# Optimization experiments

Measured on AMD Instinct MI355X. Metric: run time of the kernel, lower is better.

Reference implementation:

```python
import jax, jax.numpy as jnp
import numpy as np

H = 128  # GRU hidden size

def gru_cell(x, h, Wih, Whh, bih, bhh):
    # torch GRU gate order: r, z, n
    gx = x @ Wih.T + bih          # (B, 3H)
    gh = h @ Whh.T + bhh          # (B, 3H)
    xr, xz, xn = jnp.split(gx, 3, axis=-1)
    hr, hz, hn = jnp.split(gh, 3, axis=-1)
    r = jax.nn.sigmoid(xr + hr)
    z = jax.nn.sigmoid(xz + hz)
    n = jnp.tanh(xn + r * hn)
    return (1.0 - z) * n + z * h

def conv2d(x, w, b, stride):
    y = jax.lax.conv_general_dilated(x, w, window_strides=(stride, stride), padding='VALID',
                                     dimension_numbers=('NCHW', 'OIHW', 'NCHW'))
    return y + b[None, :, None, None]

def setup_inputs() -> dict:
    key = jax.random.key(0)
    ks = jax.random.split(key, 20)
    B, T = 8192, 64
    s = lambda *sh: 0.1
    inp = {
        'cnn_states': jax.random.normal(ks[0], (B, 8, 8, 27), jnp.float32),
        'linears_states': jax.random.normal(ks[1], (B, T, 29), jnp.float32),
        'conv1_w': jax.random.normal(ks[2], (16, 27, 3, 3), jnp.float32) * 0.1,
        'conv1_b': jnp.zeros((16,), jnp.float32),
        'conv2_w': jax.random.normal(ks[3], (32, 16, 2, 2), jnp.float32) * 0.1,
        'conv2_b': jnp.zeros((32,), jnp.float32),
        'fc_w': jax.random.normal(ks[4], (128, 128), jnp.float32) * 0.1,
        'fc_b': jnp.zeros((128,), jnp.float32),
        'enc_Wih': jax.random.normal(ks[5], (3 * H, 29), jnp.float32) * 0.1,
        'enc_Whh': jax.random.normal(ks[6], (3 * H, H), jnp.float32) * 0.1,
        'enc_bih': jnp.zeros((3 * H,), jnp.float32),
        'enc_bhh': jnp.zeros((3 * H,), jnp.float32),
        'dec_Wih': jax.random.normal(ks[7], (3 * H, H), jnp.float32) * 0.1,
        'dec_Whh': jax.random.normal(ks[8], (3 * H, H), jnp.float32) * 0.1,
        'dec_bih': jnp.zeros((3 * H,), jnp.float32),
        'dec_bhh': jnp.zeros((3 * H,), jnp.float32),
        'dis_w': jax.random.normal(ks[9], (78, 256), jnp.float32) * 0.01,
        'dis_b': jnp.zeros((78,), jnp.float32),
        'value_w': jax.random.normal(ks[10], (1, 256), jnp.float32) * 0.1,
        'value_b': jnp.zeros((1,), jnp.float32),
    }
    return inp

def _forward(cnn_states, linears_states, conv1_w, conv1_b, conv2_w, conv2_b, fc_w, fc_b,
             enc_Wih, enc_Whh, enc_bih, enc_bhh, dec_Wih, dec_Whh, dec_bih, dec_bhh,
             dis_w, dis_b, value_w, value_b):
    B, T = linears_states.shape[0], linears_states.shape[1]
    # CNN encoder (NHWC -> NCHW)
    x = jnp.transpose(cnn_states, (0, 3, 1, 2))
    x = jax.nn.relu(conv2d(x, conv1_w, conv1_b, 2))   # (B,16,3,3)
    x = jax.nn.relu(conv2d(x, conv2_w, conv2_b, 1))   # (B,32,2,2)
    x = x.reshape(B, -1)                               # (B,128), CHW order matches torch Flatten
    z_cnn = jax.nn.relu(x @ fc_w.T + fc_b)             # (B,128)

    # encoder GRU over linears_states
    xs = jnp.transpose(linears_states, (1, 0, 2))      # (T,B,29)
    h0 = jnp.zeros((B, H), linears_states.dtype)
    def enc_step(h, xt):
        h2 = gru_cell(xt, h, enc_Wih, enc_Whh, enc_bih, enc_bhh)
        return h2, None
    h_enc, _ = jax.lax.scan(enc_step, h0, xs)

    x0 = jnp.zeros((B, H), linears_states.dtype)
    def dec_step(carry, _):
        xin, h = carry
        h2 = gru_cell(xin, h, dec_Wih, dec_Whh, dec_bih, dec_bhh)
        return (h2, h2), None
    (z_pn, _), _ = jax.lax.scan(dec_step, (x0, h_enc), None, length=T)

    pn = jnp.concatenate([z_cnn, z_pn], axis=1)        # (B,256)
    distris = pn @ dis_w.T + dis_b                     # (B,78)
    value = pn @ value_w.T + value_b                   # (B,1)
    return distris, value

def reference(cnn_states, linears_states, conv1_w, conv1_b, conv2_w, conv2_b, fc_w, fc_b,
              enc_Wih, enc_Whh, enc_bih, enc_bhh, dec_Wih, dec_Whh, dec_bih, dec_bhh,
              dis_w, dis_b, value_w, value_b):
    return _forward(cnn_states, linears_states, conv1_w, conv1_b, conv2_w, conv2_b, fc_w, fc_b,
                    enc_Wih, enc_Whh, enc_bih, enc_bhh, dec_Wih, dec_Whh, dec_bih, dec_bhh,
                    dis_w, dis_b, value_w, value_b)
```

## Files before the change

### kernel.cpp

```cpp
#include <hip/hip_runtime.h>

typedef _Float16 f16;
typedef _Float16 f16x8 __attribute__((ext_vector_type(8)));
typedef float f32x4 __attribute__((ext_vector_type(4)));

#define WS_ZCNN 0
#define WS_EWIH 4194304
#define WS_EWHH 4218880
#define WS_DWC  4317184
#define WS_DWHH 4448256
#define WS_BIAS 4546560
#define WS_W1F  4550656
#define WS_W2F  4559872
#define WS_FCWF 4563968

static __device__ __forceinline__ f32x4 mfma16(f16x8 a, f16x8 b, f32x4 c) {
    return __builtin_amdgcn_mfma_f32_16x16x32_f16(a, b, c, 0, 0, 0);
}
static __device__ __forceinline__ float fexp2n(float x) {
    return __builtin_amdgcn_exp2f(x * -1.4426950408889634f);
}
static __device__ __forceinline__ void pin(f16x8& x) { asm volatile("" : "+v"(x)); }

__global__ void k_prep(const float* __restrict__ eWih, const float* __restrict__ eWhh,
                       const float* __restrict__ ebih, const float* __restrict__ ebhh,
                       const float* __restrict__ dWih, const float* __restrict__ dWhh,
                       const float* __restrict__ dbih, const float* __restrict__ dbhh,
                       const float* __restrict__ w1, const float* __restrict__ w2,
                       const float* __restrict__ fcw,
                       char* __restrict__ ws)
{
    f16* ewih = (f16*)(ws + WS_EWIH);
    f16* ewhh = (f16*)(ws + WS_EWHH);
    f16* dwc  = (f16*)(ws + WS_DWC);
    f16* dwhh = (f16*)(ws + WS_DWHH);
    float* bias = (float*)(ws + WS_BIAS);
    f16* w1f = (f16*)(ws + WS_W1F);
    f16* w2f = (f16*)(ws + WS_W2F);
    f16* fcwf = (f16*)(ws + WS_FCWF);
    const int total = 12288 + 49152 + 65536 + 49152 + 1024 + 4608 + 2048 + 16384;
    for (int i = blockIdx.x * 256 + threadIdx.x; i < total; i += gridDim.x * 256) {
        int j = i;
        if (j < 12288) { int g = j >> 5, k = j & 31;
            ewih[j] = (f16)((k < 29) ? eWih[g * 29 + k] : 0.0f); continue; }
        j -= 12288;
        if (j < 49152) { ewhh[j] = (f16)eWhh[j]; continue; }
        j -= 49152;
        if (j < 65536) { int row = j >> 7, k = j & 127; float v;
            if (row < 256)      v = dWih[row * 128 + k] + dWhh[row * 128 + k];
            else if (row < 384) v = dWih[row * 128 + k];
            else                v = dWhh[(row - 128) * 128 + k];
            dwc[j] = (f16)v; continue; }
        j -= 65536;
        if (j < 49152) { dwhh[j] = (f16)dWhh[j]; continue; }
        j -= 49152;
        if (j < 1024) {
            if (j < 256)        bias[j] = ebih[j] + ebhh[j];
            else if (j < 384)   bias[j] = ebih[j];
            else if (j < 512)   bias[j] = ebhh[j - 128];
            else if (j < 768)   bias[j] = dbih[j - 512] + dbhh[j - 512];
            else if (j < 896)   bias[j] = dbih[j - 512];
            else                bias[j] = dbhh[j - 640];
            continue; }
        j -= 1024;
        if (j < 4608) {
            int kk = j >> 9, rem = j & 511, co = rem >> 5, k = rem & 31;
            w1f[j] = (f16)((k < 27) ? w1[co * 243 + k * 9 + kk] : 0.0f); continue; }
        j -= 4608;
        if (j < 2048) {
            int s = j >> 10, rem = j & 1023, co = rem >> 5, k = rem & 31;
            int kk2 = 2 * s + (k >= 16), ci = k & 15;
            w2f[j] = (f16)w2[co * 64 + ci * 4 + kk2]; continue; }
        j -= 2048;
        fcwf[j] = (f16)fcw[j];
    }
}

__global__ __launch_bounds__(256) void k_cnn(
    const float* __restrict__ cin,
    const float* __restrict__ b1, const float* __restrict__ b2,
    const float* __restrict__ fcb,
    char* __restrict__ ws)
{
    __shared__ __align__(16) f16 a1f[16][9][24];
    __shared__ __align__(16) f16 vf[16][136];

    const int tid = threadIdx.x;
    const int base = blockIdx.x * 16;
    const f16* w1f = (const f16*)(ws + WS_W1F);
    const f16* w2f = (const f16*)(ws + WS_W2F);
    const f16* fcwf = (const f16*)(ws + WS_FCWF);
    float* z = (float*)(ws + WS_ZCNN);

    const int wv = tid >> 6, lane = tid & 63, nl = lane & 15, quad = lane >> 4;

    f16x8 bw1[9];
    #pragma unroll
    for (int kk = 0; kk < 9; kk++)
        bw1[kk] = *(const f16x8*)(w1f + (kk * 16 + nl) * 32 + quad * 8);
    float b1v = b1[nl];
    const float* imgp = cin + (size_t)(base + nl) * 1728 + quad * 8;
    for (int p = wv; p < 9; p += 4) {
        int oy = p / 3, ox = p % 3;
        f32x4 acc = {b1v, b1v, b1v, b1v};
        #pragma unroll
        for (int kk = 0; kk < 9; kk++) {
            int pix = (2 * oy + kk / 3) * 8 + (2 * ox + kk % 3);
            const float* s = imgp + pix * 27;
            f16x8 a;
            #pragma unroll
            for (int jj = 0; jj < 8; jj++) a[jj] = (f16)s[jj];
            acc = mfma16(a, bw1[kk], acc);
        }
        #pragma unroll
        for (int r = 0; r < 4; r++)
            a1f[quad * 4 + r][p][nl] = (f16)fmaxf(acc[r], 0.0f);
    }
    __syncthreads();

    {
        int y = wv >> 1, x = wv & 1;
        #pragma unroll
        for (int nt = 0; nt < 2; nt++) {
            float bv = b2[nt * 16 + nl];
            f32x4 acc = {bv, bv, bv, bv};
            #pragma unroll
            for (int s = 0; s < 2; s++) {
                int kk2 = 2 * s + (quad >> 1);
                int pos1 = (y + (kk2 >> 1)) * 3 + (x + (kk2 & 1));
                f16x8 a = *(const f16x8*)(&a1f[nl][pos1][(quad & 1) * 8]);
                f16x8 b = *(const f16x8*)(w2f + ((size_t)s * 32 + nt * 16 + nl) * 32 + quad * 8);
                acc = mfma16(a, b, acc);
            }
            #pragma unroll
            for (int r = 0; r < 4; r++)
                vf[quad * 4 + r][(nt * 16 + nl) * 4 + (y * 2 + x)] = (f16)fmaxf(acc[r], 0.0f);
        }
    }
    __syncthreads();

    #pragma unroll
    for (int nt = 0; nt < 2; nt++) {
        int o = wv * 32 + nt * 16 + nl;
        float bv = fcb[o];
        f32x4 acc = {bv, bv, bv, bv};
        #pragma unroll
        for (int kt = 0; kt < 4; kt++) {
            f16x8 a = *(const f16x8*)(&vf[nl][kt * 32 + quad * 8]);
            f16x8 b = *(const f16x8*)(fcwf + o * 128 + kt * 32 + quad * 8);
            acc = mfma16(a, b, acc);
        }
        #pragma unroll
        for (int r = 0; r < 4; r++)
            z[(size_t)(base + quad * 4 + r) * 128 + o] = fmaxf(acc[r], 0.0f);
    }
}

__global__ __launch_bounds__(512, 4) void k_gru(
    const float* __restrict__ lin,
    const char* __restrict__ ws,
    const float* __restrict__ dis_w, const float* __restrict__ dis_b,
    const float* __restrict__ value_w, const float* __restrict__ value_b,
    float* __restrict__ out)
{
    const int tid = threadIdx.x;
    const int wv = tid >> 6;
    const int lane = tid & 63;
    const int nl = lane & 15;
    const int quad = lane >> 4;
    const int j0 = wv * 16;
    const int row0 = blockIdx.x * 16;

    const f16* ewih = (const f16*)(ws + WS_EWIH);
    const f16* ewhh = (const f16*)(ws + WS_EWHH);
    const f16* dwc  = (const f16*)(ws + WS_DWC);
    const f16* dwhh = (const f16*)(ws + WS_DWHH);
    const float* bias = (const float*)(ws + WS_BIAS);
    const float* z_cnn = (const float*)(ws + WS_ZCNN);

    __shared__ __align__(16) f16 h_s[2][16][136];
    __shared__ __align__(16) f16 x_s[2][16][32];
    __shared__ __align__(16) float pn_s[16][264];

    for (int i = tid; i < 2 * 16 * 136; i += 512) ((f16*)h_s)[i] = (f16)0.0f;

    const int rsw = (nl & 8) ? 16 : 0;
    const int wrow = quad * 4;
    const int wsw = (quad >= 2) ? 16 : 0;
    const int wcol = (j0 + nl + wsw) & 127;
    const int c0 = (quad * 8 + rsw) & 127;
    const int c1 = (32 + quad * 8 + rsw) & 127;
    const int c2 = (64 + quad * 8 + rsw) & 127;
    const int c3 = (96 + quad * 8 + rsw) & 127;

    float ho[4];
    #pragma unroll
    for (int r = 0; r < 4; r++) ho[r] = 0.0f;

    const int xr = tid >> 5, xc = tid & 31;
    const bool xok = (xc < 29);
    const size_t lin_base = (size_t)(row0 + xr) * 1856 + xc;

    {
        float eb_r, eb_z, eb_xn, eb_hn;
        { int c = j0 + nl;
          eb_r = bias[c]; eb_z = bias[128 + c]; eb_xn = bias[256 + c]; eb_hn = bias[384 + c]; }
        f16x8 we_r[4], we_z[4], we_hn[4], we_xr, we_xz, we_xn;
        { int gr = j0 + nl;
          #pragma unroll
          for (int kt = 0; kt < 4; kt++) {
              we_r[kt]  = *(const f16x8*)(ewhh + gr * 128 + kt * 32 + quad * 8);
              we_z[kt]  = *(const f16x8*)(ewhh + (128 + gr) * 128 + kt * 32 + quad * 8);
              we_hn[kt] = *(const f16x8*)(ewhh + (256 + gr) * 128 + kt * 32 + quad * 8);
              pin(we_r[kt]); pin(we_z[kt]); pin(we_hn[kt]);
          }
          we_xr = *(const f16x8*)(ewih + gr * 32 + quad * 8);
          we_xz = *(const f16x8*)(ewih + (128 + gr) * 32 + quad * 8);
          we_xn = *(const f16x8*)(ewih + (256 + gr) * 32 + quad * 8);
          pin(we_xr); pin(we_xz); pin(we_xn);
        }

        float xv = xok ? lin[lin_base] : 0.0f;

#define ENC_STEP(BUF, OBUF, TN)                                                      \
        do {                                                                         \
            x_s[BUF][xr][xc] = (f16)xv;                                              \
            __syncthreads();                                                         \
            f16x8 ax = *(const f16x8*)(&x_s[BUF][nl][quad * 8]);                     \
            f16x8 ah0 = *(const f16x8*)(&h_s[BUF][nl][c0]);                          \
            f16x8 ah1 = *(const f16x8*)(&h_s[BUF][nl][c1]);                          \
            f16x8 ah2 = *(const f16x8*)(&h_s[BUF][nl][c2]);                          \
            f16x8 ah3 = *(const f16x8*)(&h_s[BUF][nl][c3]);                          \
            if ((TN) < 64) xv = xok ? lin[lin_base + (TN) * 29] : 0.0f;              \
            f32x4 aR  = {eb_r, eb_r, eb_r, eb_r};                                    \
            f32x4 aZ  = {eb_z, eb_z, eb_z, eb_z};                                    \
            f32x4 aXN = {eb_xn, eb_xn, eb_xn, eb_xn};                                \
            f32x4 aHN = {eb_hn, eb_hn, eb_hn, eb_hn};                                \
            aR  = mfma16(ax, we_xr, aR);                                             \
            aZ  = mfma16(ax, we_xz, aZ);                                             \
            aXN = mfma16(ax, we_xn, aXN);                                            \
            aR  = mfma16(ah0, we_r[0], aR);  aR  = mfma16(ah1, we_r[1], aR);         \
            aR  = mfma16(ah2, we_r[2], aR);  aR  = mfma16(ah3, we_r[3], aR);         \
            aZ  = mfma16(ah0, we_z[0], aZ);  aZ  = mfma16(ah1, we_z[1], aZ);         \
            aZ  = mfma16(ah2, we_z[2], aZ);  aZ  = mfma16(ah3, we_z[3], aZ);         \
            aHN = mfma16(ah0, we_hn[0], aHN); aHN = mfma16(ah1, we_hn[1], aHN);      \
            aHN = mfma16(ah2, we_hn[2], aHN); aHN = mfma16(ah3, we_hn[3], aHN);      \
            _Pragma("unroll")                                                        \
            for (int r = 0; r < 4; r++) {                                            \
                float ea = fexp2n(aR[r]), eb = fexp2n(aZ[r]);                        \
                float s1 = 1.0f + ea, s2 = 1.0f + eb;                                \
                float R = __builtin_amdgcn_rcpf(s1 * s2);                            \
                float rg = s2 * R, zg = s1 * R;                                      \
                float ec = fexp2n(2.0f * (aXN[r] + rg * aHN[r]));                    \
                float ng = (1.0f - ec) * __builtin_amdgcn_rcpf(1.0f + ec);           \
                float h = (1.0f - zg) * ng + zg * ho[r];                             \
                ho[r] = h;                                                           \
                h_s[OBUF][wrow + r][wcol] = (f16)h;                                  \
            }                                                                        \
        } while (0)

        for (int t = 0; t < 64; t += 2) {
            ENC_STEP(0, 1, t + 1);
            ENC_STEP(1, 0, t + 2);
        }
#undef ENC_STEP
    }

    float db_r, db_z, db_xn, db_hn;
    { int c = j0 + nl;
      db_r = bias[512 + c]; db_z = bias[640 + c]; db_xn = bias[768 + c]; db_hn = bias[896 + c]; }

    {
        __syncthreads();
        f16x8 ah0 = *(const f16x8*)(&h_s[0][nl][c0]);
        f16x8 ah1 = *(const f16x8*)(&h_s[0][nl][c1]);
        f16x8 ah2 = *(const f16x8*)(&h_s[0][nl][c2]);
        f16x8 ah3 = *(const f16x8*)(&h_s[0][nl][c3]);
        int gr = j0 + nl;
        f32x4 aR  = {db_r, db_r, db_r, db_r};
        f32x4 aZ  = {db_z, db_z, db_z, db_z};
        f32x4 aHN = {db_hn, db_hn, db_hn, db_hn};
        #pragma unroll
        for (int kt = 0; kt < 4; kt++) {
            f16x8 b0 = *(const f16x8*)(dwhh + gr * 128 + kt * 32 + quad * 8);
            f16x8 b1 = *(const f16x8*)(dwhh + (128 + gr) * 128 + kt * 32 + quad * 8);
            f16x8 b2 = *(const f16x8*)(dwhh + (256 + gr) * 128 + kt * 32 + quad * 8);
            f16x8 a = (kt == 0) ? ah0 : (kt == 1) ? ah1 : (kt == 2) ? ah2 : ah3;
            aR  = mfma16(a, b0, aR);
            aZ  = mfma16(a, b1, aZ);
            aHN = mfma16(a, b2, aHN);
        }
        #pragma unroll
        for (int r = 0; r < 4; r++) {
            float ea = fexp2n(aR[r]), eb = fexp2n(aZ[r]);
            float s1 = 1.0f + ea, s2 = 1.0f + eb;
            float R = __builtin_amdgcn_rcpf(s1 * s2);
            float rg = s2 * R, zg = s1 * R;
            float ec = fexp2n(2.0f * (db_xn + rg * aHN[r]));
            float ng = (1.0f - ec) * __builtin_amdgcn_rcpf(1.0f + ec);
            float h = (1.0f - zg) * ng + zg * ho[r];
            ho[r] = h;
            h_s[1][wrow + r][wcol] = (f16)h;
        }
    }
    {
        f16x8 wd_r[4], wd_z[4], wd_xn[4], wd_hn[4];
        { int gr = j0 + nl;
          #pragma unroll
          for (int kt = 0; kt < 4; kt++) {
              wd_r[kt]  = *(const f16x8*)(dwc + gr * 128 + kt * 32 + quad * 8);
              wd_z[kt]  = *(const f16x8*)(dwc + (128 + gr) * 128 + kt * 32 + quad * 8);
              wd_xn[kt] = *(const f16x8*)(dwc + (256 + gr) * 128 + kt * 32 + quad * 8);
              wd_hn[kt] = *(const f16x8*)(dwc + (384 + gr) * 128 + kt * 32 + quad * 8);
              pin(wd_r[kt]); pin(wd_z[kt]); pin(wd_xn[kt]); pin(wd_hn[kt]);
          }
        }

#define DEC_STEP(BUF, OBUF)                                                          \
        do {                                                                         \
            __syncthreads();                                                         \
            f16x8 ah0 = *(const f16x8*)(&h_s[BUF][nl][c0]);                          \
            f16x8 ah1 = *(const f16x8*)(&h_s[BUF][nl][c1]);                          \
            f16x8 ah2 = *(const f16x8*)(&h_s[BUF][nl][c2]);                          \
            f16x8 ah3 = *(const f16x8*)(&h_s[BUF][nl][c3]);                          \
            f32x4 aR  = {db_r, db_r, db_r, db_r};                                    \
            f32x4 aZ  = {db_z, db_z, db_z, db_z};                                    \
            f32x4 aXN = {db_xn, db_xn, db_xn, db_xn};                                \
            f32x4 aHN = {db_hn, db_hn, db_hn, db_hn};                                \
            aR  = mfma16(ah0, wd_r[0], aR);   aR  = mfma16(ah1, wd_r[1], aR);        \
            aR  = mfma16(ah2, wd_r[2], aR);   aR  = mfma16(ah3, wd_r[3], aR);        \
            aZ  = mfma16(ah0, wd_z[0], aZ);   aZ  = mfma16(ah1, wd_z[1], aZ);        \
            aZ  = mfma16(ah2, wd_z[2], aZ);   aZ  = mfma16(ah3, wd_z[3], aZ);        \
            aXN = mfma16(ah0, wd_xn[0], aXN); aXN = mfma16(ah1, wd_xn[1], aXN);      \
            aXN = mfma16(ah2, wd_xn[2], aXN); aXN = mfma16(ah3, wd_xn[3], aXN);      \
            aHN = mfma16(ah0, wd_hn[0], aHN); aHN = mfma16(ah1, wd_hn[1], aHN);      \
            aHN = mfma16(ah2, wd_hn[2], aHN); aHN = mfma16(ah3, wd_hn[3], aHN);      \
            _Pragma("unroll")                                                        \
            for (int r = 0; r < 4; r++) {                                            \
                float ea = fexp2n(aR[r]), eb = fexp2n(aZ[r]);                        \
                float s1 = 1.0f + ea, s2 = 1.0f + eb;                                \
                float R = __builtin_amdgcn_rcpf(s1 * s2);                            \
                float rg = s2 * R, zg = s1 * R;                                      \
                float ec = fexp2n(2.0f * (aXN[r] + rg * aHN[r]));                    \
                float ng = (1.0f - ec) * __builtin_amdgcn_rcpf(1.0f + ec);           \
                float h = (1.0f - zg) * ng + zg * ho[r];                             \
                ho[r] = h;                                                           \
                h_s[OBUF][wrow + r][wcol] = (f16)h;                                  \
            }                                                                        \
        } while (0)

        DEC_STEP(1, 0);
        for (int t = 2; t < 64; t += 2) {
            DEC_STEP(0, 1);
            DEC_STEP(1, 0);
        }
#undef DEC_STEP
    }

    #pragma unroll
    for (int r = 0; r < 4; r++)
        pn_s[wrow + r][128 + j0 + nl] = ho[r];
    for (int i = tid; i < 16 * 128; i += 512) {
        int rr = i >> 7, cc = i & 127;
        pn_s[rr][cc] = z_cnn[(size_t)(row0 + rr) * 128 + cc];
    }
    __syncthreads();

    const int rr = tid & 15, og = tid >> 4;
    const float4* pr4 = (const float4*)(&pn_s[rr][0]);
    for (int o = og; o < 79; o += 32) {
        const float* wrow_p = (o < 78) ? (dis_w + o * 256) : value_w;
        float acc = (o < 78) ? dis_b[o] : value_b[0];
        const float4* wr4 = (const float4*)wrow_p;
        #pragma unroll 8
        for (int k = 0; k < 64; k++) {
            float4 a = wr4[k], b = pr4[k];
            acc += a.x * b.x + a.y * b.y + a.z * b.z + a.w * b.w;
        }
        if (o < 78) out[(size_t)(row0 + rr) * 78 + o] = acc;
        else        out[(size_t)8192 * 78 + row0 + rr] = acc;
    }
}

extern "C" void kernel_launch(void* const* d_in, const int* in_sizes, int n_in,
                              void* d_out, int out_size, void* d_ws, size_t ws_size,
                              hipStream_t stream)
{
    (void)in_sizes; (void)n_in; (void)out_size; (void)ws_size;
    const float* cnn  = (const float*)d_in[0];
    const float* lin  = (const float*)d_in[1];
    const float* c1w  = (const float*)d_in[2];
    const float* c1b  = (const float*)d_in[3];
    const float* c2w  = (const float*)d_in[4];
    const float* c2b  = (const float*)d_in[5];
    const float* fcw  = (const float*)d_in[6];
    const float* fcb  = (const float*)d_in[7];
    const float* eWih = (const float*)d_in[8];
    const float* eWhh = (const float*)d_in[9];
    const float* ebih = (const float*)d_in[10];
    const float* ebhh = (const float*)d_in[11];
    const float* dWih = (const float*)d_in[12];
    const float* dWhh = (const float*)d_in[13];
    const float* dbih = (const float*)d_in[14];
    const float* dbhh = (const float*)d_in[15];
    const float* disw = (const float*)d_in[16];
    const float* disb = (const float*)d_in[17];
    const float* vw   = (const float*)d_in[18];
    const float* vb   = (const float*)d_in[19];
    char* ws = (char*)d_ws;
    float* out = (float*)d_out;

    hipLaunchKernelGGL(k_prep, dim3(128), dim3(256), 0, stream,
                       eWih, eWhh, ebih, ebhh, dWih, dWhh, dbih, dbhh,
                       c1w, c2w, fcw, ws);
    hipLaunchKernelGGL(k_cnn, dim3(512), dim3(256), 0, stream,
                       cnn, c1b, c2b, fcb, ws);
    hipLaunchKernelGGL(k_gru, dim3(512), dim3(512), 0, stream,
                       lin, ws, disw, disb, vw, vb, out);
}
```

Before: 350.0 us.

## Fuse CNN branch into GRU kernel and write CNN features directly to shared memory

The separate CNN kernel is folded into the start of the GRU kernel. Its conv1, conv2 and fc stages run over 8 waves with aliased shared memory, and the fc output is written straight into the pn_s buffer, which removes the global round trip of z_cnn and one kernel launch. The asm register-pinning barriers on the weight fragments are dropped, and the GRU state update is rewritten as ng + z*(h-ng) to save an operation. The cost is that CNN work now adds latency to each GRU block, and conv1 uses only 9 of 8x2 wave slots, which leaves some waves idle. It also risks different register allocation in the GRU loop now that the pins are gone.

```diff
diff --git a/kernel.cpp b/kernel.cpp
--- a/kernel.cpp
+++ b/kernel.cpp
@@ -4,7 +4,6 @@
 typedef _Float16 f16x8 __attribute__((ext_vector_type(8)));
 typedef float f32x4 __attribute__((ext_vector_type(4)));
 
-#define WS_ZCNN 0
 #define WS_EWIH 4194304
 #define WS_EWHH 4218880
 #define WS_DWC  4317184
@@ -20,7 +19,6 @@
 static __device__ __forceinline__ float fexp2n(float x) {
     return __builtin_amdgcn_exp2f(x * -1.4426950408889634f);
 }
-static __device__ __forceinline__ void pin(f16x8& x) { asm volatile("" : "+v"(x)); }
 
 __global__ void k_prep(const float* __restrict__ eWih, const float* __restrict__ eWhh,
                        const float* __restrict__ ebih, const float* __restrict__ ebhh,
@@ -76,52 +74,64 @@
     }
 }
 
-__global__ __launch_bounds__(256) void k_cnn(
+__global__ __launch_bounds__(512, 4) void k_gru(
     const float* __restrict__ cin,
+    const float* __restrict__ lin,
     const float* __restrict__ b1, const float* __restrict__ b2,
     const float* __restrict__ fcb,
-    char* __restrict__ ws)
+    const char* __restrict__ ws,
+    const float* __restrict__ dis_w, const float* __restrict__ dis_b,
+    const float* __restrict__ value_w, const float* __restrict__ value_b,
+    float* __restrict__ out)
 {
-    __shared__ __align__(16) f16 a1f[16][9][24];
-    __shared__ __align__(16) f16 vf[16][136];
+    __shared__ __align__(16) char smem[32000];
+    f16 (*h_s)[16][136]  = (f16(*)[16][136])(smem);
+    f16 (*x_s)[16][32]   = (f16(*)[16][32])(smem + 8704);
+    float (*pn_s)[264]   = (float(*)[264])(smem + 10752);
+    f16 (*a1f)[9][24]    = (f16(*)[9][24])(smem);
+    f16 (*vf)[136]       = (f16(*)[136])(smem + 27648);
 
     const int tid = threadIdx.x;
-    const int base = blockIdx.x * 16;
+    const int wv = tid >> 6;
+    const int lane = tid & 63;
+    const int nl = lane & 15;
+    const int quad = lane >> 4;
+    const int j0 = wv * 16;
+    const int row0 = blockIdx.x * 16;
+
+    const f16* ewih = (const f16*)(ws + WS_EWIH);
+    const f16* ewhh = (const f16*)(ws + WS_EWHH);
+    const f16* dwc  = (const f16*)(ws + WS_DWC);
+    const f16* dwhh = (const f16*)(ws + WS_DWHH);
+    const float* bias = (const float*)(ws + WS_BIAS);
     const f16* w1f = (const f16*)(ws + WS_W1F);
     const f16* w2f = (const f16*)(ws + WS_W2F);
     const f16* fcwf = (const f16*)(ws + WS_FCWF);
-    float* z = (float*)(ws + WS_ZCNN);
-
-    const int wv = tid >> 6, lane = tid & 63, nl = lane & 15, quad = lane >> 4;
-
-    f16x8 bw1[9];
-    #pragma unroll
-    for (int kk = 0; kk < 9; kk++)
-        bw1[kk] = *(const f16x8*)(w1f + (kk * 16 + nl) * 32 + quad * 8);
-    float b1v = b1[nl];
-    const float* imgp = cin + (size_t)(base + nl) * 1728 + quad * 8;
-    for (int p = wv; p < 9; p += 4) {
-        int oy = p / 3, ox = p % 3;
-        f32x4 acc = {b1v, b1v, b1v, b1v};
-        #pragma unroll
-        for (int kk = 0; kk < 9; kk++) {
-            int pix = (2 * oy + kk / 3) * 8 + (2 * ox + kk % 3);
-            const float* s = imgp + pix * 27;
-            f16x8 a;
-            #pragma unroll
-            for (int jj = 0; jj < 8; jj++) a[jj] = (f16)s[jj];
-            acc = mfma16(a, bw1[kk], acc);
-        }
-        #pragma unroll
-        for (int r = 0; r < 4; r++)
-            a1f[quad * 4 + r][p][nl] = (f16)fmaxf(acc[r], 0.0f);
-    }
-    __syncthreads();
 
     {
-        int y = wv >> 1, x = wv & 1;
-        #pragma unroll
-        for (int nt = 0; nt < 2; nt++) {
+        const float* imgp = cin + (size_t)(row0 + nl) * 1728 + quad * 8;
+        float b1v = b1[nl];
+        for (int p = wv; p < 9; p += 8) {
+            int oy = p / 3, ox = p % 3;
+            f32x4 acc = {b1v, b1v, b1v, b1v};
+            #pragma unroll
+            for (int kk = 0; kk < 9; kk++) {
+                f16x8 bw = *(const f16x8*)(w1f + (kk * 16 + nl) * 32 + quad * 8);
+                int pix = (2 * oy + kk / 3) * 8 + (2 * ox + kk % 3);
+                const float* s = imgp + pix * 27;
+                f16x8 a;
+                #pragma unroll
+                for (int jj = 0; jj < 8; jj++) a[jj] = (f16)s[jj];
+                acc = mfma16(a, bw, acc);
+            }
+            #pragma unroll
+            for (int r = 0; r < 4; r++)
+                a1f[quad * 4 + r][p][nl] = (f16)fmaxf(acc[r], 0.0f);
+        }
+        __syncthreads();
+        {
+            int pos = wv >> 1, nt = wv & 1;
+            int y = pos >> 1, x = pos & 1;
             float bv = b2[nt * 16 + nl];
             f32x4 acc = {bv, bv, bv, bv};
             #pragma unroll
@@ -136,51 +146,23 @@
             for (int r = 0; r < 4; r++)
                 vf[quad * 4 + r][(nt * 16 + nl) * 4 + (y * 2 + x)] = (f16)fmaxf(acc[r], 0.0f);
         }
-    }
-    __syncthreads();
-
-    #pragma unroll
-    for (int nt = 0; nt < 2; nt++) {
-        int o = wv * 32 + nt * 16 + nl;
-        float bv = fcb[o];
-        f32x4 acc = {bv, bv, bv, bv};
-        #pragma unroll
-        for (int kt = 0; kt < 4; kt++) {
-            f16x8 a = *(const f16x8*)(&vf[nl][kt * 32 + quad * 8]);
-            f16x8 b = *(const f16x8*)(fcwf + o * 128 + kt * 32 + quad * 8);
-            acc = mfma16(a, b, acc);
-        }
-        #pragma unroll
-        for (int r = 0; r < 4; r++)
-            z[(size_t)(base + quad * 4 + r) * 128 + o] = fmaxf(acc[r], 0.0f);
-    }
-}
-
-__global__ __launch_bounds__(512, 4) void k_gru(
-    const float* __restrict__ lin,
-    const char* __restrict__ ws,
-    const float* __restrict__ dis_w, const float* __restrict__ dis_b,
-    const float* __restrict__ value_w, const float* __restrict__ value_b,
-    float* __restrict__ out)
-{
-    const int tid = threadIdx.x;
-    const int wv = tid >> 6;
-    const int lane = tid & 63;
-    const int nl = lane & 15;
-    const int quad = lane >> 4;
-    const int j0 = wv * 16;
-    const int row0 = blockIdx.x * 16;
-
-    const f16* ewih = (const f16*)(ws + WS_EWIH);
-    const f16* ewhh = (const f16*)(ws + WS_EWHH);
-    const f16* dwc  = (const f16*)(ws + WS_DWC);
-    const f16* dwhh = (const f16*)(ws + WS_DWHH);
-    const float* bias = (const float*)(ws + WS_BIAS);
-    const float* z_cnn = (const float*)(ws + WS_ZCNN);
-
-    __shared__ __align__(16) f16 h_s[2][16][136];
-    __shared__ __align__(16) f16 x_s[2][16][32];
-    __shared__ __align__(16) float pn_s[16][264];
+        __syncthreads();
+        {
+            int o = wv * 16 + nl;
+            float bv = fcb[o];
+            f32x4 acc = {bv, bv, bv, bv};
+            #pragma unroll
+            for (int kt = 0; kt < 4; kt++) {
+                f16x8 a = *(const f16x8*)(&vf[nl][kt * 32 + quad * 8]);
+                f16x8 b = *(const f16x8*)(fcwf + o * 128 + kt * 32 + quad * 8);
+                acc = mfma16(a, b, acc);
+            }
+            #pragma unroll
+            for (int r = 0; r < 4; r++)
+                pn_s[quad * 4 + r][o] = fmaxf(acc[r], 0.0f);
+        }
+        __syncthreads();
+    }
 
     for (int i = tid; i < 2 * 16 * 136; i += 512) ((f16*)h_s)[i] = (f16)0.0f;
 
@@ -212,12 +194,10 @@
               we_r[kt]  = *(const f16x8*)(ewhh + gr * 128 + kt * 32 + quad * 8);
               we_z[kt]  = *(const f16x8*)(ewhh + (128 + gr) * 128 + kt * 32 + quad * 8);
               we_hn[kt] = *(const f16x8*)(ewhh + (256 + gr) * 128 + kt * 32 + quad * 8);
-              pin(we_r[kt]); pin(we_z[kt]); pin(we_hn[kt]);
           }
           we_xr = *(const f16x8*)(ewih + gr * 32 + quad * 8);
           we_xz = *(const f16x8*)(ewih + (128 + gr) * 32 + quad * 8);
           we_xn = *(const f16x8*)(ewih + (256 + gr) * 32 + quad * 8);
-          pin(we_xr); pin(we_xz); pin(we_xn);
         }
 
         float xv = xok ? lin[lin_base] : 0.0f;
@@ -253,7 +233,7 @@
                 float rg = s2 * R, zg = s1 * R;                                      \
                 float ec = fexp2n(2.0f * (aXN[r] + rg * aHN[r]));                    \
                 float ng = (1.0f - ec) * __builtin_amdgcn_rcpf(1.0f + ec);           \
-                float h = (1.0f - zg) * ng + zg * ho[r];                             \
+                float h = ng + zg * (ho[r] - ng);                                    \
                 ho[r] = h;                                                           \
                 h_s[OBUF][wrow + r][wcol] = (f16)h;                                  \
             }                                                                        \
@@ -298,7 +278,7 @@
             float rg = s2 * R, zg = s1 * R;
             float ec = fexp2n(2.0f * (db_xn + rg * aHN[r]));
             float ng = (1.0f - ec) * __builtin_amdgcn_rcpf(1.0f + ec);
-            float h = (1.0f - zg) * ng + zg * ho[r];
+            float h = ng + zg * (ho[r] - ng);
             ho[r] = h;
             h_s[1][wrow + r][wcol] = (f16)h;
         }
@@ -312,7 +292,6 @@
               wd_z[kt]  = *(const f16x8*)(dwc + (128 + gr) * 128 + kt * 32 + quad * 8);
               wd_xn[kt] = *(const f16x8*)(dwc + (256 + gr) * 128 + kt * 32 + quad * 8);
               wd_hn[kt] = *(const f16x8*)(dwc + (384 + gr) * 128 + kt * 32 + quad * 8);
-              pin(wd_r[kt]); pin(wd_z[kt]); pin(wd_xn[kt]); pin(wd_hn[kt]);
           }
         }
 
@@ -343,7 +322,7 @@
                 float rg = s2 * R, zg = s1 * R;                                      \
                 float ec = fexp2n(2.0f * (aXN[r] + rg * aHN[r]));                    \
                 float ng = (1.0f - ec) * __builtin_amdgcn_rcpf(1.0f + ec);           \
-                float h = (1.0f - zg) * ng + zg * ho[r];                             \
+                float h = ng + zg * (ho[r] - ng);                                    \
                 ho[r] = h;                                                           \
                 h_s[OBUF][wrow + r][wcol] = (f16)h;                                  \
             }                                                                        \
@@ -360,10 +339,6 @@
     #pragma unroll
     for (int r = 0; r < 4; r++)
         pn_s[wrow + r][128 + j0 + nl] = ho[r];
-    for (int i = tid; i < 16 * 128; i += 512) {
-        int rr = i >> 7, cc = i & 127;
-        pn_s[rr][cc] = z_cnn[(size_t)(row0 + rr) * 128 + cc];
-    }
     __syncthreads();
 
     const int rr = tid & 15, og = tid >> 4;
@@ -413,8 +388,6 @@
     hipLaunchKernelGGL(k_prep, dim3(128), dim3(256), 0, stream,
                        eWih, eWhh, ebih, ebhh, dWih, dWhh, dbih, dbhh,
                        c1w, c2w, fcw, ws);
-    hipLaunchKernelGGL(k_cnn, dim3(512), dim3(256), 0, stream,
-                       cnn, c1b, c2b, fcb, ws);
     hipLaunchKernelGGL(k_gru, dim3(512), dim3(512), 0, stream,
-                       lin, ws, disw, disb, vw, vb, out);
-}
+                       cnn, lin, c1b, c2b, fcb, ws, disw, disb, vw, vb, out);
+}
```

Measured after the change: 332.2 us, median of 2. 5.1% less time.
